# Performance work log

Measured on AMD Instinct MI355X. Metric: run time of the kernel, lower is better.

Reference implementation:

```python
import jax, jax.numpy as jnp
import numpy as np

B, S, D, H, DO, E, K = 4, 2048, 1024, 4096, 1024, 8, 2


def setup_inputs() -> dict:
    key = jax.random.key(0)
    ks = jax.random.split(key, 5)
    sD = 1.0 / np.sqrt(D)
    sH = 1.0 / np.sqrt(H)
    return {
        "x": jax.random.normal(ks[0], (B, S, D), jnp.float32),
        "gate_w": jax.random.normal(ks[1], (D, E), jnp.float32) * sD,
        "gate_b": jnp.zeros((E,), jnp.float32),
        "w1": jax.random.normal(ks[2], (E, D, H), jnp.float32) * sD,
        "b1": jnp.zeros((E, H), jnp.float32),
        "w2": jax.random.normal(ks[3], (E, H, DO), jnp.float32) * sH,
        "b2": jnp.zeros((E, DO), jnp.float32),
    }


def reference(x, gate_w, gate_b, w1, b1, w2, b2):
    # Eval mode: no gating noise, dropout is identity.
    T = B * S
    xf = x.reshape(T, D)
    logits = xf @ gate_w + gate_b                      # [T, E]
    top_v, top_i = jax.lax.top_k(logits, K)            # [T, K]
    top_w = jax.nn.softmax(top_v, axis=-1)             # softmax over top-k scores
    # scatter top-k weights into dense [T, E] gate weights (indices are distinct)
    weights = jnp.zeros_like(logits).at[jnp.arange(T)[:, None], top_i].set(top_w)
    # dense per-expert MLP, combined with (mostly zero) gate weights —
    # same math as the masked gather/scatter loop in the torch source
    h = jax.nn.relu(jnp.einsum('td,edh->teh', xf, w1) + b1)   # [T, E, H]
    eo = jnp.einsum('teh,eho->teo', h, w2) + b2               # [T, E, DO]
    out = jnp.einsum('te,teo->to', weights, eo).reshape(B, S, DO)
    expert_usage = jnp.bincount(top_i.reshape(-1), length=E)
    return out, weights, expert_usage, top_i
```

## Files before the change

kernel.cpp:

```cpp
#include <hip/hip_runtime.h>
#include <cstdint>
#include <cstddef>

typedef unsigned short u16;
typedef unsigned int u32;
typedef short s16x8 __attribute__((ext_vector_type(8)));
typedef float f32x4 __attribute__((ext_vector_type(4)));

#define T_TOK 8192
#define D_IN  1024
#define H_DIM 4096
#define DO_DIM 1024

__device__ __forceinline__ u16 f2bf(float f) {
    u32 u = __float_as_uint(f);
    return (u16)((u + 0x7FFFu + ((u >> 16) & 1u)) >> 16);
}

__device__ __forceinline__ f32x4 mfma16(s16x8 a, s16x8 b, f32x4 c) {
    return __builtin_amdgcn_mfma_f32_16x16x32_bf16(a, b, c, 0, 0, 0);
}

__device__ __forceinline__ void gload16(const void* g, void* l) {
    __builtin_amdgcn_global_load_lds(
        (const __attribute__((address_space(1))) void*)g,
        (__attribute__((address_space(3))) void*)l,
        16, 0, 0);
}

__global__ __launch_bounds__(256) void gate_kernel(
    const float* __restrict__ x, const float* __restrict__ gw,
    const float* __restrict__ gb, float* __restrict__ weights_out,
    float* __restrict__ topi_out, int* __restrict__ gcounts,
    int* __restrict__ tok_list, int* __restrict__ slot_of_tok)
{
    const int wid = threadIdx.x >> 6;
    const int lane = threadIdx.x & 63;
    const int tbase = blockIdx.x << 4;
    __shared__ int lcount[8];
    __shared__ int gbase[8];
    __shared__ short tinfo[16][4];
    if (threadIdx.x < 8) lcount[threadIdx.x] = 0;
    __syncthreads();

    for (int j = 0; j < 4; ++j) {
        const int t = tbase + (wid << 2) + j;
        const float* xr = x + ((size_t)t << 10);
        float p[8];
#pragma unroll
        for (int e = 0; e < 8; ++e) p[e] = 0.f;
#pragma unroll
        for (int i = 0; i < 16; ++i) {
            int d = lane + i * 64;
            float xv = xr[d];
            const f32x4 g0 = *(const f32x4*)(gw + d * 8);
            const f32x4 g1 = *(const f32x4*)(gw + d * 8 + 4);
            p[0] += xv * g0[0]; p[1] += xv * g0[1]; p[2] += xv * g0[2]; p[3] += xv * g0[3];
            p[4] += xv * g1[0]; p[5] += xv * g1[1]; p[6] += xv * g1[2]; p[7] += xv * g1[3];
        }
#pragma unroll
        for (int off = 32; off >= 1; off >>= 1) {
#pragma unroll
            for (int e = 0; e < 8; ++e) p[e] += __shfl_xor(p[e], off, 64);
        }
        if (lane == 0) {
            float lg[8];
#pragma unroll
            for (int e = 0; e < 8; ++e) lg[e] = p[e] + gb[e];
            int i0 = 0;
            for (int e = 1; e < 8; ++e) if (lg[e] > lg[i0]) i0 = e;
            int i1 = (i0 == 0) ? 1 : 0;
            for (int e = 0; e < 8; ++e) if (e != i0 && lg[e] > lg[i1]) i1 = e;
            float ex = expf(lg[i1] - lg[i0]);
            float p0 = 1.f / (1.f + ex);
            float p1 = ex / (1.f + ex);
#pragma unroll
            for (int e = 0; e < 8; ++e)
                weights_out[t * 8 + e] = (e == i0) ? p0 : ((e == i1) ? p1 : 0.f);
            topi_out[t * 2 + 0] = (float)i0;
            topi_out[t * 2 + 1] = (float)i1;
            int idx = (wid << 2) + j;
            int r0 = atomicAdd(&lcount[i0], 1);
            int r1 = atomicAdd(&lcount[i1], 1);
            tinfo[idx][0] = (short)i0; tinfo[idx][1] = (short)r0;
            tinfo[idx][2] = (short)i1; tinfo[idx][3] = (short)r1;
        }
    }
    __syncthreads();
    if (threadIdx.x < 8)
        gbase[threadIdx.x] = atomicAdd(&gcounts[threadIdx.x * 32], lcount[threadIdx.x]);
    __syncthreads();
    if (threadIdx.x < 16) {
        int t = tbase + threadIdx.x;
        int i0 = tinfo[threadIdx.x][0], r0 = tinfo[threadIdx.x][1];
        int i1 = tinfo[threadIdx.x][2], r1 = tinfo[threadIdx.x][3];
        int pos0 = gbase[i0] + r0;
        int pos1 = gbase[i1] + r1;
        tok_list[(i0 << 13) + pos0] = t;
        slot_of_tok[t * 2 + 0] = (i0 << 13) | pos0;
        tok_list[(i1 << 13) + pos1] = t;
        slot_of_tok[t * 2 + 1] = (i1 << 13) | pos1;
    }
}

__global__ void zero_counts_kernel(int* c) { c[threadIdx.x] = 0; }

__global__ void scan_kernel(const int* __restrict__ gcounts, int* __restrict__ counts,
                            int* __restrict__ base, float* __restrict__ usage_out,
                            int* __restrict__ rbt) {
    if (threadIdx.x == 0) {
        int acc = 0;
        for (int e = 0; e < 8; ++e) {
            int c = gcounts[e * 32];
            counts[e] = c;
            base[e] = acc;
            acc += c;
            usage_out[e] = (float)c;
        }
        int nrb = 0;
        for (int e = 0; e < 8; ++e) {
            int nb = (counts[e] + 127) >> 7;
            for (int rb = 0; rb < nb; ++rb) rbt[1 + nrb++] = (e << 16) | rb;
        }
        rbt[0] = nrb;
    }
}

__global__ __launch_bounds__(256) void gather_kernel(
    const float* __restrict__ x, const int* __restrict__ slot_of_tok,
    const int* __restrict__ base, u16* __restrict__ xg)
{
    const int t = blockIdx.x;
    const int s = slot_of_tok[t * 2 + blockIdx.y];
    const int slot = base[s >> 13] + (s & 8191);
    const int d = threadIdx.x * 4;
    float4 v = *(const float4*)(x + ((size_t)t << 10) + d);
    ushort4 h;
    h.x = f2bf(v.x); h.y = f2bf(v.y); h.z = f2bf(v.z); h.w = f2bf(v.w);
    *(ushort4*)(xg + ((size_t)slot << 10) + d) = h;
}

__global__ __launch_bounds__(256) void transpose_kernel(
    const float* __restrict__ w1, const float* __restrict__ w2,
    u16* __restrict__ w1t, u16* __restrict__ w2t, int chunk, int HC)
{
    const int e = blockIdx.z;
    const int tid = threadIdx.x;
    const int tiles_h = HC >> 6;
    const int ntile1 = 16 * tiles_h;
    int b = blockIdx.x;
    const float* src; u16* dst;
    size_t sstride, dstride;
    int r0, c0;
    if (b < ntile1) {
        int tr = b / tiles_h, tc = b % tiles_h;
        r0 = tr * 64; c0 = tc * 64;
        src = w1 + (size_t)e * D_IN * H_DIM + (size_t)chunk * HC;
        sstride = H_DIM;
        dst = w1t + (size_t)e * HC * D_IN;
        dstride = D_IN;
    } else {
        int tb = b - ntile1;
        int tr = tb / 16, tc = tb % 16;
        r0 = tr * 64; c0 = tc * 64;
        src = w2 + ((size_t)e * H_DIM + (size_t)chunk * HC) * DO_DIM;
        sstride = DO_DIM;
        dst = w2t + (size_t)e * DO_DIM * HC;
        dstride = HC;
    }
    __shared__ u16 tile[64][68];
#pragma unroll
    for (int i = 0; i < 4; ++i) {
        int flat = i * 1024 + tid * 4;
        int rr = flat >> 6, cc = flat & 63;
        float4 v = *(const float4*)(src + (size_t)(r0 + rr) * sstride + c0 + cc);
        ushort4 h4;
        h4.x = f2bf(v.x); h4.y = f2bf(v.y); h4.z = f2bf(v.z); h4.w = f2bf(v.w);
        *(ushort4*)&tile[rr][cc] = h4;
    }
    __syncthreads();
#pragma unroll
    for (int i = 0; i < 4; ++i) {
        int flat = i * 1024 + tid * 4;
        int rr = flat >> 6, cc = flat & 63;
        ushort4 o;
        o.x = tile[cc + 0][rr]; o.y = tile[cc + 1][rr];
        o.z = tile[cc + 2][rr]; o.w = tile[cc + 3][rr];
        *(ushort4*)(dst + (size_t)(c0 + rr) * dstride + r0 + cc) = o;
    }
}


__device__ __forceinline__ void stage6s(const char* const gA[2], const char* const gB[4],
                                        char* slab, int koff, int tid) {
    char* l = slab + __builtin_amdgcn_readfirstlane((tid >> 6) << 10);
#pragma unroll
    for (int i = 0; i < 2; ++i) gload16(gA[i] + koff, l + i * 8192);
#pragma unroll
    for (int i = 0; i < 4; ++i) gload16(gB[i] + koff, l + 16384 + i * 8192);
}

#define GEMM_CORE(NTV) \
    const int arow = (wm << 6) + (lane & 15); \
    const int brow = (wn << 6) + (lane & 15); \
    const int ko = (lane >> 4) << 4; \
    const int aoff0 = arow * 128 + (ko ^ ((arow & 7) << 4)); \
    const int aoff1 = arow * 128 + ((64 + ko) ^ ((arow & 7) << 4)); \
    const int boff0 = 16384 + brow * 128 + (ko ^ ((brow & 7) << 4)); \
    const int boff1 = 16384 + brow * 128 + ((64 + ko) ^ ((brow & 7) << 4)); \
    f32x4 acc[4][4]; \
    _Pragma("unroll") \
    for (int m = 0; m < 4; ++m) \
        _Pragma("unroll") \
        for (int n = 0; n < 4; ++n) acc[m][n] = f32x4{0.f, 0.f, 0.f, 0.f}; \
    stage6s(gA, gB, sm, 0, tid); \
    stage6s(gA, gB, sm + 49152, 128, tid); \
    int cs = 0; \
    _Pragma("unroll 1") \
    for (int t = 0; t < (NTV); ++t) { \
        if (t + 1 < (NTV)) asm volatile("s_waitcnt vmcnt(6)" ::: "memory"); \
        else               asm volatile("s_waitcnt vmcnt(0)" ::: "memory"); \
        __builtin_amdgcn_sched_barrier(0); \
        __builtin_amdgcn_s_barrier(); \
        __builtin_amdgcn_sched_barrier(0); \
        if (t + 2 < (NTV)) { \
            int ss = cs + 2; if (ss >= 3) ss -= 3; \
            stage6s(gA, gB, sm + ss * 49152, (t + 2) * 128, tid); \
        } \
        const char* S = sm + cs * 49152; \
        s16x8 la0[4], lb0[4], la1[4], lb1[4]; \
        _Pragma("unroll") \
        for (int m = 0; m < 4; ++m) la0[m] = *(const s16x8*)(S + aoff0 + m * 2048); \
        _Pragma("unroll") \
        for (int n = 0; n < 4; ++n) lb0[n] = *(const s16x8*)(S + boff0 + n * 2048); \
        _Pragma("unroll") \
        for (int m = 0; m < 4; ++m) la1[m] = *(const s16x8*)(S + aoff1 + m * 2048); \
        _Pragma("unroll") \
        for (int n = 0; n < 4; ++n) lb1[n] = *(const s16x8*)(S + boff1 + n * 2048); \
        __builtin_amdgcn_s_setprio(1); \
        _Pragma("unroll") \
        for (int m = 0; m < 4; ++m) \
            _Pragma("unroll") \
            for (int n = 0; n < 4; ++n) acc[m][n] = mfma16(la0[m], lb0[n], acc[m][n]); \
        _Pragma("unroll") \
        for (int m = 0; m < 4; ++m) \
            _Pragma("unroll") \
            for (int n = 0; n < 4; ++n) acc[m][n] = mfma16(la1[m], lb1[n], acc[m][n]); \
        __builtin_amdgcn_s_setprio(0); \
        cs = cs + 1; if (cs == 3) cs = 0; \
    }

__global__ __launch_bounds__(512) void gemm1_kernel(
    const u16* __restrict__ xg, const u16* __restrict__ w1t,
    const float* __restrict__ b1, u16* __restrict__ hbuf,
    const int* __restrict__ counts, const int* __restrict__ base,
    const int* __restrict__ rbt, int chunk, int HC)
{
    const int nrb = rbt[0];
    if (blockIdx.y >= nrb) return;
    const int ent = rbt[1 + blockIdx.y];
    const int e = ent >> 16;
    const int row0 = (ent & 0xffff) << 7;
    const int n_e = counts[e];
    const int sbase = base[e];
    const int col0 = blockIdx.x << 8;
    const int tid = threadIdx.x;
    const int lane = tid & 63;
    const int wv = tid >> 6;
    const int wm = wv >> 2;
    const int wn = wv & 3;

    __shared__ char sm[147456];

    const int srow_ = tid >> 3;
    const int scb_  = ((tid & 7) << 4) ^ ((srow_ & 7) << 4);
    const char* gA[2]; const char* gB[4];
#pragma unroll
    for (int i = 0; i < 2; ++i) {
        int slot = sbase + row0 + i * 64 + srow_;
        slot = slot < 16383 ? slot : 16383;
        gA[i] = (const char*)xg + ((size_t)slot << 11) + scb_;
    }
#pragma unroll
    for (int i = 0; i < 4; ++i) {
        int hrow = col0 + i * 64 + srow_;
        gB[i] = (const char*)w1t + (((size_t)e * HC + hrow) << 11) + scb_;
    }

    GEMM_CORE(16)

    const int crow = (wm << 6) + ((lane >> 4) << 2);
    const int ccol = (wn << 6) + (lane & 15);
    float bias_n[4];
#pragma unroll
    for (int n = 0; n < 4; ++n)
        bias_n[n] = b1[(e << 12) + chunk * HC + col0 + ccol + n * 16];
#pragma unroll
    for (int m = 0; m < 4; ++m) {
#pragma unroll
        for (int j = 0; j < 4; ++j) {
            int r = row0 + crow + m * 16 + j;
            if (r < n_e) {
                u16* dst = hbuf + (size_t)(sbase + r) * HC + col0;
#pragma unroll
                for (int n = 0; n < 4; ++n) {
                    float v = acc[m][n][j] + bias_n[n];
                    v = v > 0.f ? v : 0.f;
                    dst[ccol + n * 16] = f2bf(v);
                }
            }
        }
    }
}

__global__ __launch_bounds__(512) void gemm2_kernel(
    const u16* __restrict__ hbuf, const u16* __restrict__ w2t,
    const float* __restrict__ b2, float* __restrict__ eo,
    const int* __restrict__ counts, const int* __restrict__ base,
    const int* __restrict__ rbt, int chunk, int HC)
{
    const int nrb = rbt[0];
    if (blockIdx.y >= nrb) return;
    const int ent = rbt[1 + blockIdx.y];
    const int e = ent >> 16;
    const int row0 = (ent & 0xffff) << 7;
    const int n_e = counts[e];
    const int sbase = base[e];
    const int col0 = blockIdx.x << 8;
    const int tid = threadIdx.x;
    const int lane = tid & 63;
    const int wv = tid >> 6;
    const int wm = wv >> 2;
    const int wn = wv & 3;

    __shared__ char sm[147456];

    const int srow_ = tid >> 3;
    const int scb_  = ((tid & 7) << 4) ^ ((srow_ & 7) << 4);
    const char* gA[2]; const char* gB[4];
#pragma unroll
    for (int i = 0; i < 2; ++i) {
        int slot = sbase + row0 + i * 64 + srow_;
        slot = slot < 16383 ? slot : 16383;
        gA[i] = (const char*)hbuf + (((size_t)slot * HC) << 1) + scb_;
    }
#pragma unroll
    for (int i = 0; i < 4; ++i) {
        int orow = col0 + i * 64 + srow_;
        gB[i] = (const char*)w2t + ((((size_t)(e << 10) + orow) * HC) << 1) + scb_;
    }

    const int NT = HC >> 6;
    GEMM_CORE(NT)

    const int crow = (wm << 6) + ((lane >> 4) << 2);
    const int ccol = (wn << 6) + (lane & 15);
    float bias_n[4];
#pragma unroll
    for (int n = 0; n < 4; ++n)
        bias_n[n] = (chunk == 0) ? b2[(e << 10) + col0 + ccol + n * 16] : 0.f;
#pragma unroll
    for (int m = 0; m < 4; ++m) {
#pragma unroll
        for (int j = 0; j < 4; ++j) {
            int r = row0 + crow + m * 16 + j;
            if (r < n_e) {
                float* dst = eo + ((size_t)(sbase + r) << 10) + col0;
#pragma unroll
                for (int n = 0; n < 4; ++n) {
                    int c = ccol + n * 16;
                    float v = acc[m][n][j] + bias_n[n];
                    if (chunk) v += dst[c];
                    dst[c] = v;
                }
            }
        }
    }
}

__global__ __launch_bounds__(256) void combine_kernel(
    const float* __restrict__ eo, const float* __restrict__ weights,
    const int* __restrict__ slot_of_tok, const int* __restrict__ base,
    float* __restrict__ out)
{
    const int t = blockIdx.x;
    const int tid = threadIdx.x;
    int s0 = slot_of_tok[t * 2], s1 = slot_of_tok[t * 2 + 1];
    int e0 = s0 >> 13, e1 = s1 >> 13;
    int c0 = base[e0] + (s0 & 8191);
    int c1 = base[e1] + (s1 & 8191);
    float w0 = weights[t * 8 + e0];
    float w1 = weights[t * 8 + e1];
    int c = tid * 4;
    f32x4 a = *(const f32x4*)(eo + ((size_t)c0 << 10) + c);
    f32x4 b = *(const f32x4*)(eo + ((size_t)c1 << 10) + c);
    f32x4 r;
    r[0] = w0 * a[0] + w1 * b[0];
    r[1] = w0 * a[1] + w1 * b[1];
    r[2] = w0 * a[2] + w1 * b[2];
    r[3] = w0 * a[3] + w1 * b[3];
    *(f32x4*)(out + ((size_t)t << 10) + c) = r;
}

extern "C" void kernel_launch(void* const* d_in, const int* in_sizes, int n_in,
                              void* d_out, int out_size, void* d_ws, size_t ws_size,
                              hipStream_t stream)
{
    const float* x      = (const float*)d_in[0];
    const float* gate_w = (const float*)d_in[1];
    const float* gate_b = (const float*)d_in[2];
    const float* w1     = (const float*)d_in[3];
    const float* b1     = (const float*)d_in[4];
    const float* w2     = (const float*)d_in[5];
    const float* b2     = (const float*)d_in[6];

    float* out         = (float*)d_out;
    float* weights_out = out + (size_t)T_TOK * DO_DIM;
    float* usage_out   = weights_out + (size_t)T_TOK * 8;
    float* topi_out    = usage_out + 8;

    char* p = (char*)d_ws;
    int* gcounts = (int*)p;      p += 1024;
    int* counts = (int*)p;       p += 256;
    int* base   = (int*)p;       p += 256;
    int* rbt    = (int*)p;       p += 1024;
    int* tok_list = (int*)p;     p += (size_t)8 * 8192 * 4;
    int* slot_of_tok = (int*)p;  p += (size_t)8192 * 2 * 4;
    const size_t fixed = (size_t)(p - (char*)d_ws);

    const size_t xg_bytes = (size_t)16384 * 1024 * 2;
    const size_t eo_bytes = (size_t)16384 * 1024 * 4;
    int HC;
    if      (ws_size >= fixed + xg_bytes + eo_bytes + (size_t)65536 * 4096) HC = 4096;
    else if (ws_size >= fixed + xg_bytes + eo_bytes + (size_t)65536 * 2048) HC = 2048;
    else if (ws_size >= fixed + xg_bytes + eo_bytes + (size_t)65536 * 1024) HC = 1024;
    else                                                                    HC = 512;

    u16* xg   = (u16*)p; p += xg_bytes;
    u16* w1t  = (u16*)p; p += (size_t)8 * HC * 1024 * 2;
    u16* w2t  = (u16*)p; p += (size_t)8 * 1024 * HC * 2;
    u16* hbuf = (u16*)p; p += (size_t)16384 * HC * 2;
    float* eo = (float*)p;

    zero_counts_kernel<<<1, 256, 0, stream>>>(gcounts);
    gate_kernel<<<T_TOK / 16, 256, 0, stream>>>(x, gate_w, gate_b, weights_out, topi_out,
                                                gcounts, tok_list, slot_of_tok);
    scan_kernel<<<1, 64, 0, stream>>>(gcounts, counts, base, usage_out, rbt);
    gather_kernel<<<dim3(T_TOK, 2), 256, 0, stream>>>(x, slot_of_tok, base, xg);

    const int NC = H_DIM / HC;
    for (int c = 0; c < NC; ++c) {
        int tiles_h = HC / 64;
        transpose_kernel<<<dim3(2 * 16 * tiles_h, 1, 8), 256, 0, stream>>>(w1, w2, w1t, w2t, c, HC);
        gemm1_kernel<<<dim3(HC / 256, 136, 1), 512, 0, stream>>>(xg, w1t, b1, hbuf,
                                                                 counts, base, rbt, c, HC);
        gemm2_kernel<<<dim3(DO_DIM / 256, 136, 1), 512, 0, stream>>>(hbuf, w2t, b2, eo,
                                                                     counts, base, rbt, c, HC);
    }
    combine_kernel<<<T_TOK, 256, 0, stream>>>(eo, weights_out, slot_of_tok, base, out);
}
```

Baseline: 513.2 us.

## Fuse token gather into GEMM1 A-loads and merge gating with weight transpose

GEMM1 now reads fp32 activation rows directly from x through tok_list, converts them to bf16 in registers and writes them into LDS. This replaces the separate gather kernel and the bf16 xg buffer. The gate kernel and the first-chunk weight transpose are merged into one launch, with the block index choosing the role. This removes a kernel launch and the round trip of gathered activations through memory. The cost is a GEMM1 pipeline that mixes register-staged A loads with async B loads, reads twice the A bytes in fp32, and needs hand-tuned waitcnt values.

```diff
diff --git a/kernel.cpp b/kernel.cpp
--- a/kernel.cpp
+++ b/kernel.cpp
@@ -15,6 +15,15 @@
 __device__ __forceinline__ u16 f2bf(float f) {
     u32 u = __float_as_uint(f);
     return (u16)((u + 0x7FFFu + ((u >> 16) & 1u)) >> 16);
+}
+
+__device__ __forceinline__ s16x8 pack8(float4 a, float4 b) {
+    s16x8 r;
+    r[0] = (short)f2bf(a.x); r[1] = (short)f2bf(a.y);
+    r[2] = (short)f2bf(a.z); r[3] = (short)f2bf(a.w);
+    r[4] = (short)f2bf(b.x); r[5] = (short)f2bf(b.y);
+    r[6] = (short)f2bf(b.z); r[7] = (short)f2bf(b.w);
+    return r;
 }
 
 __device__ __forceinline__ f32x4 mfma16(s16x8 a, s16x8 b, f32x4 c) {
@@ -28,127 +37,95 @@
         16, 0, 0);
 }
 
-__global__ __launch_bounds__(256) void gate_kernel(
+__global__ __launch_bounds__(256) void gate_transpose_kernel(
     const float* __restrict__ x, const float* __restrict__ gw,
     const float* __restrict__ gb, float* __restrict__ weights_out,
     float* __restrict__ topi_out, int* __restrict__ gcounts,
-    int* __restrict__ tok_list, int* __restrict__ slot_of_tok)
+    int* __restrict__ tok_list, int* __restrict__ slot_of_tok,
+    const float* __restrict__ w1, const float* __restrict__ w2,
+    u16* __restrict__ w1t, u16* __restrict__ w2t,
+    int chunk, int HC, int gate_blocks)
 {
-    const int wid = threadIdx.x >> 6;
-    const int lane = threadIdx.x & 63;
-    const int tbase = blockIdx.x << 4;
+    __shared__ u16 tile[64][68];
     __shared__ int lcount[8];
     __shared__ int gbase[8];
     __shared__ short tinfo[16][4];
-    if (threadIdx.x < 8) lcount[threadIdx.x] = 0;
-    __syncthreads();
-
-    for (int j = 0; j < 4; ++j) {
-        const int t = tbase + (wid << 2) + j;
-        const float* xr = x + ((size_t)t << 10);
-        float p[8];
-#pragma unroll
-        for (int e = 0; e < 8; ++e) p[e] = 0.f;
-#pragma unroll
-        for (int i = 0; i < 16; ++i) {
-            int d = lane + i * 64;
-            float xv = xr[d];
-            const f32x4 g0 = *(const f32x4*)(gw + d * 8);
-            const f32x4 g1 = *(const f32x4*)(gw + d * 8 + 4);
-            p[0] += xv * g0[0]; p[1] += xv * g0[1]; p[2] += xv * g0[2]; p[3] += xv * g0[3];
-            p[4] += xv * g1[0]; p[5] += xv * g1[1]; p[6] += xv * g1[2]; p[7] += xv * g1[3];
-        }
-#pragma unroll
-        for (int off = 32; off >= 1; off >>= 1) {
-#pragma unroll
-            for (int e = 0; e < 8; ++e) p[e] += __shfl_xor(p[e], off, 64);
-        }
-        if (lane == 0) {
-            float lg[8];
-#pragma unroll
-            for (int e = 0; e < 8; ++e) lg[e] = p[e] + gb[e];
-            int i0 = 0;
-            for (int e = 1; e < 8; ++e) if (lg[e] > lg[i0]) i0 = e;
-            int i1 = (i0 == 0) ? 1 : 0;
-            for (int e = 0; e < 8; ++e) if (e != i0 && lg[e] > lg[i1]) i1 = e;
-            float ex = expf(lg[i1] - lg[i0]);
-            float p0 = 1.f / (1.f + ex);
-            float p1 = ex / (1.f + ex);
-#pragma unroll
-            for (int e = 0; e < 8; ++e)
-                weights_out[t * 8 + e] = (e == i0) ? p0 : ((e == i1) ? p1 : 0.f);
-            topi_out[t * 2 + 0] = (float)i0;
-            topi_out[t * 2 + 1] = (float)i1;
-            int idx = (wid << 2) + j;
-            int r0 = atomicAdd(&lcount[i0], 1);
-            int r1 = atomicAdd(&lcount[i1], 1);
-            tinfo[idx][0] = (short)i0; tinfo[idx][1] = (short)r0;
-            tinfo[idx][2] = (short)i1; tinfo[idx][3] = (short)r1;
-        }
-    }
-    __syncthreads();
-    if (threadIdx.x < 8)
-        gbase[threadIdx.x] = atomicAdd(&gcounts[threadIdx.x * 32], lcount[threadIdx.x]);
-    __syncthreads();
-    if (threadIdx.x < 16) {
-        int t = tbase + threadIdx.x;
-        int i0 = tinfo[threadIdx.x][0], r0 = tinfo[threadIdx.x][1];
-        int i1 = tinfo[threadIdx.x][2], r1 = tinfo[threadIdx.x][3];
-        int pos0 = gbase[i0] + r0;
-        int pos1 = gbase[i1] + r1;
-        tok_list[(i0 << 13) + pos0] = t;
-        slot_of_tok[t * 2 + 0] = (i0 << 13) | pos0;
-        tok_list[(i1 << 13) + pos1] = t;
-        slot_of_tok[t * 2 + 1] = (i1 << 13) | pos1;
-    }
-}
-
-__global__ void zero_counts_kernel(int* c) { c[threadIdx.x] = 0; }
-
-__global__ void scan_kernel(const int* __restrict__ gcounts, int* __restrict__ counts,
-                            int* __restrict__ base, float* __restrict__ usage_out,
-                            int* __restrict__ rbt) {
-    if (threadIdx.x == 0) {
-        int acc = 0;
-        for (int e = 0; e < 8; ++e) {
-            int c = gcounts[e * 32];
-            counts[e] = c;
-            base[e] = acc;
-            acc += c;
-            usage_out[e] = (float)c;
-        }
-        int nrb = 0;
-        for (int e = 0; e < 8; ++e) {
-            int nb = (counts[e] + 127) >> 7;
-            for (int rb = 0; rb < nb; ++rb) rbt[1 + nrb++] = (e << 16) | rb;
-        }
-        rbt[0] = nrb;
-    }
-}
-
-__global__ __launch_bounds__(256) void gather_kernel(
-    const float* __restrict__ x, const int* __restrict__ slot_of_tok,
-    const int* __restrict__ base, u16* __restrict__ xg)
-{
-    const int t = blockIdx.x;
-    const int s = slot_of_tok[t * 2 + blockIdx.y];
-    const int slot = base[s >> 13] + (s & 8191);
-    const int d = threadIdx.x * 4;
-    float4 v = *(const float4*)(x + ((size_t)t << 10) + d);
-    ushort4 h;
-    h.x = f2bf(v.x); h.y = f2bf(v.y); h.z = f2bf(v.z); h.w = f2bf(v.w);
-    *(ushort4*)(xg + ((size_t)slot << 10) + d) = h;
-}
-
-__global__ __launch_bounds__(256) void transpose_kernel(
-    const float* __restrict__ w1, const float* __restrict__ w2,
-    u16* __restrict__ w1t, u16* __restrict__ w2t, int chunk, int HC)
-{
-    const int e = blockIdx.z;
+
+    const int bid = blockIdx.x;
+    if (bid < gate_blocks) {
+        const int wid = threadIdx.x >> 6;
+        const int lane = threadIdx.x & 63;
+        const int tbase = bid << 4;
+        if (threadIdx.x < 8) lcount[threadIdx.x] = 0;
+        __syncthreads();
+        for (int j = 0; j < 4; ++j) {
+            const int t = tbase + (wid << 2) + j;
+            const float* xr = x + ((size_t)t << 10);
+            float p[8];
+#pragma unroll
+            for (int e = 0; e < 8; ++e) p[e] = 0.f;
+#pragma unroll
+            for (int i = 0; i < 16; ++i) {
+                int d = lane + i * 64;
+                float xv = xr[d];
+                const f32x4 g0 = *(const f32x4*)(gw + d * 8);
+                const f32x4 g1 = *(const f32x4*)(gw + d * 8 + 4);
+                p[0] += xv * g0[0]; p[1] += xv * g0[1]; p[2] += xv * g0[2]; p[3] += xv * g0[3];
+                p[4] += xv * g1[0]; p[5] += xv * g1[1]; p[6] += xv * g1[2]; p[7] += xv * g1[3];
+            }
+#pragma unroll
+            for (int off = 32; off >= 1; off >>= 1) {
+#pragma unroll
+                for (int e = 0; e < 8; ++e) p[e] += __shfl_xor(p[e], off, 64);
+            }
+            if (lane == 0) {
+                float lg[8];
+#pragma unroll
+                for (int e = 0; e < 8; ++e) lg[e] = p[e] + gb[e];
+                int i0 = 0;
+                for (int e = 1; e < 8; ++e) if (lg[e] > lg[i0]) i0 = e;
+                int i1 = (i0 == 0) ? 1 : 0;
+                for (int e = 0; e < 8; ++e) if (e != i0 && lg[e] > lg[i1]) i1 = e;
+                float ex = expf(lg[i1] - lg[i0]);
+                float p0 = 1.f / (1.f + ex);
+                float p1 = ex / (1.f + ex);
+#pragma unroll
+                for (int e = 0; e < 8; ++e)
+                    weights_out[t * 8 + e] = (e == i0) ? p0 : ((e == i1) ? p1 : 0.f);
+                topi_out[t * 2 + 0] = (float)i0;
+                topi_out[t * 2 + 1] = (float)i1;
+                int idx = (wid << 2) + j;
+                int r0 = atomicAdd(&lcount[i0], 1);
+                int r1 = atomicAdd(&lcount[i1], 1);
+                tinfo[idx][0] = (short)i0; tinfo[idx][1] = (short)r0;
+                tinfo[idx][2] = (short)i1; tinfo[idx][3] = (short)r1;
+            }
+        }
+        __syncthreads();
+        if (threadIdx.x < 8)
+            gbase[threadIdx.x] = atomicAdd(&gcounts[threadIdx.x * 32], lcount[threadIdx.x]);
+        __syncthreads();
+        if (threadIdx.x < 16) {
+            int t = tbase + threadIdx.x;
+            int i0 = tinfo[threadIdx.x][0], r0 = tinfo[threadIdx.x][1];
+            int i1 = tinfo[threadIdx.x][2], r1 = tinfo[threadIdx.x][3];
+            int pos0 = gbase[i0] + r0;
+            int pos1 = gbase[i1] + r1;
+            tok_list[(i0 << 13) + pos0] = t;
+            slot_of_tok[t * 2 + 0] = (i0 << 13) | pos0;
+            tok_list[(i1 << 13) + pos1] = t;
+            slot_of_tok[t * 2 + 1] = (i1 << 13) | pos1;
+        }
+        return;
+    }
+
     const int tid = threadIdx.x;
     const int tiles_h = HC >> 6;
+    const int per_e = 32 * tiles_h;
     const int ntile1 = 16 * tiles_h;
-    int b = blockIdx.x;
+    const int b2 = bid - gate_blocks;
+    const int e = b2 / per_e;
+    const int b = b2 - e * per_e;
     const float* src; u16* dst;
     size_t sstride, dstride;
     int r0, c0;
@@ -168,7 +145,6 @@
         dst = w2t + (size_t)e * DO_DIM * HC;
         dstride = HC;
     }
-    __shared__ u16 tile[64][68];
 #pragma unroll
     for (int i = 0; i < 4; ++i) {
         int flat = i * 1024 + tid * 4;
@@ -190,6 +166,29 @@
     }
 }
 
+__global__ void zero_counts_kernel(int* c) { c[threadIdx.x] = 0; }
+
+__global__ void scan_kernel(const int* __restrict__ gcounts, int* __restrict__ counts,
+                            int* __restrict__ base, float* __restrict__ usage_out,
+                            int* __restrict__ rbt) {
+    if (threadIdx.x == 0) {
+        int acc = 0;
+        for (int e = 0; e < 8; ++e) {
+            int c = gcounts[e * 32];
+            counts[e] = c;
+            base[e] = acc;
+            acc += c;
+            usage_out[e] = (float)c;
+        }
+        int nrb = 0;
+        for (int e = 0; e < 8; ++e) {
+            int nb = (counts[e] + 127) >> 7;
+            for (int rb = 0; rb < nb; ++rb) rbt[1 + nrb++] = (e << 16) | rb;
+        }
+        rbt[0] = nrb;
+    }
+}
+
 
 __device__ __forceinline__ void stage6s(const char* const gA[2], const char* const gB[4],
                                         char* slab, int koff, int tid) {
@@ -200,61 +199,60 @@
     for (int i = 0; i < 4; ++i) gload16(gB[i] + koff, l + 16384 + i * 8192);
 }
 
-#define GEMM_CORE(NTV) \
-    const int arow = (wm << 6) + (lane & 15); \
-    const int brow = (wn << 6) + (lane & 15); \
-    const int ko = (lane >> 4) << 4; \
-    const int aoff0 = arow * 128 + (ko ^ ((arow & 7) << 4)); \
-    const int aoff1 = arow * 128 + ((64 + ko) ^ ((arow & 7) << 4)); \
-    const int boff0 = 16384 + brow * 128 + (ko ^ ((brow & 7) << 4)); \
-    const int boff1 = 16384 + brow * 128 + ((64 + ko) ^ ((brow & 7) << 4)); \
-    f32x4 acc[4][4]; \
+#define MFMA_BLOCK(S) do { \
+    s16x8 la0[4], lb0[4], la1[4], lb1[4]; \
+    _Pragma("unroll") \
+    for (int m = 0; m < 4; ++m) la0[m] = *(const s16x8*)((S) + aoff0 + m * 2048); \
+    _Pragma("unroll") \
+    for (int n = 0; n < 4; ++n) lb0[n] = *(const s16x8*)((S) + boff0 + n * 2048); \
+    _Pragma("unroll") \
+    for (int m = 0; m < 4; ++m) la1[m] = *(const s16x8*)((S) + aoff1 + m * 2048); \
+    _Pragma("unroll") \
+    for (int n = 0; n < 4; ++n) lb1[n] = *(const s16x8*)((S) + boff1 + n * 2048); \
+    __builtin_amdgcn_s_setprio(1); \
     _Pragma("unroll") \
     for (int m = 0; m < 4; ++m) \
         _Pragma("unroll") \
-        for (int n = 0; n < 4; ++n) acc[m][n] = f32x4{0.f, 0.f, 0.f, 0.f}; \
-    stage6s(gA, gB, sm, 0, tid); \
-    stage6s(gA, gB, sm + 49152, 128, tid); \
-    int cs = 0; \
-    _Pragma("unroll 1") \
-    for (int t = 0; t < (NTV); ++t) { \
-        if (t + 1 < (NTV)) asm volatile("s_waitcnt vmcnt(6)" ::: "memory"); \
-        else               asm volatile("s_waitcnt vmcnt(0)" ::: "memory"); \
-        __builtin_amdgcn_sched_barrier(0); \
-        __builtin_amdgcn_s_barrier(); \
-        __builtin_amdgcn_sched_barrier(0); \
-        if (t + 2 < (NTV)) { \
-            int ss = cs + 2; if (ss >= 3) ss -= 3; \
-            stage6s(gA, gB, sm + ss * 49152, (t + 2) * 128, tid); \
-        } \
-        const char* S = sm + cs * 49152; \
-        s16x8 la0[4], lb0[4], la1[4], lb1[4]; \
+        for (int n = 0; n < 4; ++n) acc[m][n] = mfma16(la0[m], lb0[n], acc[m][n]); \
+    _Pragma("unroll") \
+    for (int m = 0; m < 4; ++m) \
         _Pragma("unroll") \
-        for (int m = 0; m < 4; ++m) la0[m] = *(const s16x8*)(S + aoff0 + m * 2048); \
-        _Pragma("unroll") \
-        for (int n = 0; n < 4; ++n) lb0[n] = *(const s16x8*)(S + boff0 + n * 2048); \
-        _Pragma("unroll") \
-        for (int m = 0; m < 4; ++m) la1[m] = *(const s16x8*)(S + aoff1 + m * 2048); \
-        _Pragma("unroll") \
-        for (int n = 0; n < 4; ++n) lb1[n] = *(const s16x8*)(S + boff1 + n * 2048); \
-        __builtin_amdgcn_s_setprio(1); \
-        _Pragma("unroll") \
-        for (int m = 0; m < 4; ++m) \
-            _Pragma("unroll") \
-            for (int n = 0; n < 4; ++n) acc[m][n] = mfma16(la0[m], lb0[n], acc[m][n]); \
-        _Pragma("unroll") \
-        for (int m = 0; m < 4; ++m) \
-            _Pragma("unroll") \
-            for (int n = 0; n < 4; ++n) acc[m][n] = mfma16(la1[m], lb1[n], acc[m][n]); \
-        __builtin_amdgcn_s_setprio(0); \
-        cs = cs + 1; if (cs == 3) cs = 0; \
-    }
+        for (int n = 0; n < 4; ++n) acc[m][n] = mfma16(la1[m], lb1[n], acc[m][n]); \
+    __builtin_amdgcn_s_setprio(0); } while(0)
+
+#define G1BODY(TAU, LD, CV) do { \
+    if ((TAU) + 1 < 16) asm volatile("s_waitcnt vmcnt(4)" ::: "memory"); \
+    else                asm volatile("s_waitcnt vmcnt(0)" ::: "memory"); \
+    asm volatile("s_waitcnt lgkmcnt(0)" ::: "memory"); \
+    __builtin_amdgcn_sched_barrier(0); \
+    __builtin_amdgcn_s_barrier(); \
+    __builtin_amdgcn_sched_barrier(0); \
+    int s1_ = cs + 1; if (s1_ == 3) s1_ = 0; \
+    int s2_ = cs + 2; if (s2_ >= 3) s2_ -= 3; \
+    if ((TAU) + 2 < 16) { \
+        const int ka_ = ((TAU) + 2) << 8; \
+        LD##0 = *(const float4*)(gAx0 + ka_);      LD##1 = *(const float4*)(gAx0 + ka_ + 16); \
+        LD##2 = *(const float4*)(gAx1 + ka_);      LD##3 = *(const float4*)(gAx1 + ka_ + 16); \
+        const int kb_ = ((TAU) + 2) << 7; \
+        char* l_ = sm + s2_ * 49152 + 16384 + wofs; \
+        gload16(gB[0] + kb_, l_);           gload16(gB[1] + kb_, l_ + 8192); \
+        gload16(gB[2] + kb_, l_ + 16384);   gload16(gB[3] + kb_, l_ + 24576); \
+    } \
+    if ((TAU) + 1 < 16) { \
+        char* sw_ = sm + s1_ * 49152; \
+        *(s16x8*)(sw_ + wA0) = pack8(CV##0, CV##1); \
+        *(s16x8*)(sw_ + wA1) = pack8(CV##2, CV##3); \
+    } \
+    const char* S_ = sm + cs * 49152; \
+    MFMA_BLOCK(S_); \
+    cs = s1_; } while(0)
 
 __global__ __launch_bounds__(512) void gemm1_kernel(
-    const u16* __restrict__ xg, const u16* __restrict__ w1t,
+    const float* __restrict__ x, const u16* __restrict__ w1t,
     const float* __restrict__ b1, u16* __restrict__ hbuf,
     const int* __restrict__ counts, const int* __restrict__ base,
-    const int* __restrict__ rbt, int chunk, int HC)
+    const int* __restrict__ rbt, const int* __restrict__ tok_list,
+    int chunk, int HC)
 {
     const int nrb = rbt[0];
     if (blockIdx.y >= nrb) return;
@@ -272,22 +270,63 @@
 
     __shared__ char sm[147456];
 
-    const int srow_ = tid >> 3;
-    const int scb_  = ((tid & 7) << 4) ^ ((srow_ & 7) << 4);
-    const char* gA[2]; const char* gB[4];
-#pragma unroll
-    for (int i = 0; i < 2; ++i) {
-        int slot = sbase + row0 + i * 64 + srow_;
-        slot = slot < 16383 ? slot : 16383;
-        gA[i] = (const char*)xg + ((size_t)slot << 11) + scb_;
-    }
+    const int r0_ = tid >> 3;
+    const int r1_ = r0_ + 64;
+    const int kseg = tid & 7;
+    int row_a0 = row0 + r0_; row_a0 = row_a0 < n_e ? row_a0 : n_e - 1;
+    int row_a1 = row0 + r1_; row_a1 = row_a1 < n_e ? row_a1 : n_e - 1;
+    const int tk0 = tok_list[(e << 13) + row_a0];
+    const int tk1 = tok_list[(e << 13) + row_a1];
+    const char* gAx0 = (const char*)x + ((size_t)tk0 << 12) + (kseg << 5);
+    const char* gAx1 = (const char*)x + ((size_t)tk1 << 12) + (kseg << 5);
+    const int wA0 = r0_ * 128 + ((kseg << 4) ^ ((r0_ & 7) << 4));
+    const int wA1 = r1_ * 128 + ((kseg << 4) ^ ((r1_ & 7) << 4));
+
+    const int scb_ = ((tid & 7) << 4) ^ (((tid >> 3) & 7) << 4);
+    const char* gB[4];
 #pragma unroll
     for (int i = 0; i < 4; ++i) {
-        int hrow = col0 + i * 64 + srow_;
+        int hrow = col0 + i * 64 + (tid >> 3);
         gB[i] = (const char*)w1t + (((size_t)e * HC + hrow) << 11) + scb_;
     }
-
-    GEMM_CORE(16)
+    const int wofs = __builtin_amdgcn_readfirstlane((tid >> 6) << 10);
+
+    const int arow = (wm << 6) + (lane & 15);
+    const int brow = (wn << 6) + (lane & 15);
+    const int ko = (lane >> 4) << 4;
+    const int aoff0 = arow * 128 + (ko ^ ((arow & 7) << 4));
+    const int aoff1 = arow * 128 + ((64 + ko) ^ ((arow & 7) << 4));
+    const int boff0 = 16384 + brow * 128 + (ko ^ ((brow & 7) << 4));
+    const int boff1 = 16384 + brow * 128 + ((64 + ko) ^ ((brow & 7) << 4));
+
+    f32x4 acc[4][4];
+#pragma unroll
+    for (int m = 0; m < 4; ++m)
+#pragma unroll
+        for (int n = 0; n < 4; ++n) acc[m][n] = f32x4{0.f, 0.f, 0.f, 0.f};
+
+    float4 aE0, aE1, aE2, aE3, aO0, aO1, aO2, aO3;
+
+    aE0 = *(const float4*)(gAx0);       aE1 = *(const float4*)(gAx0 + 16);
+    aE2 = *(const float4*)(gAx1);       aE3 = *(const float4*)(gAx1 + 16);
+    {   char* l_ = sm + 16384 + wofs;
+        gload16(gB[0], l_);           gload16(gB[1], l_ + 8192);
+        gload16(gB[2], l_ + 16384);   gload16(gB[3], l_ + 24576); }
+    aO0 = *(const float4*)(gAx0 + 256); aO1 = *(const float4*)(gAx0 + 272);
+    aO2 = *(const float4*)(gAx1 + 256); aO3 = *(const float4*)(gAx1 + 272);
+    {   char* l_ = sm + 49152 + 16384 + wofs;
+        gload16(gB[0] + 128, l_);           gload16(gB[1] + 128, l_ + 8192);
+        gload16(gB[2] + 128, l_ + 16384);   gload16(gB[3] + 128, l_ + 24576); }
+    asm volatile("s_waitcnt vmcnt(12)" ::: "memory");
+    *(s16x8*)(sm + wA0) = pack8(aE0, aE1);
+    *(s16x8*)(sm + wA1) = pack8(aE2, aE3);
+
+    int cs = 0;
+#pragma unroll 1
+    for (int tt = 0; tt < 16; tt += 2) {
+        G1BODY(tt, aE, aO);
+        G1BODY(tt + 1, aO, aE);
+    }
 
     const int crow = (wm << 6) + ((lane >> 4) << 2);
     const int ccol = (wn << 6) + (lane & 15);
@@ -335,23 +374,56 @@
 
     __shared__ char sm[147456];
 
-    const int srow_ = tid >> 3;
-    const int scb_  = ((tid & 7) << 4) ^ ((srow_ & 7) << 4);
+    const int scb_ = ((tid & 7) << 4) ^ (((tid >> 3) & 7) << 4);
     const char* gA[2]; const char* gB[4];
 #pragma unroll
     for (int i = 0; i < 2; ++i) {
-        int slot = sbase + row0 + i * 64 + srow_;
+        int slot = sbase + row0 + i * 64 + (tid >> 3);
         slot = slot < 16383 ? slot : 16383;
         gA[i] = (const char*)hbuf + (((size_t)slot * HC) << 1) + scb_;
     }
 #pragma unroll
     for (int i = 0; i < 4; ++i) {
-        int orow = col0 + i * 64 + srow_;
+        int orow = col0 + i * 64 + (tid >> 3);
         gB[i] = (const char*)w2t + ((((size_t)(e << 10) + orow) * HC) << 1) + scb_;
     }
+    const int wofs = __builtin_amdgcn_readfirstlane((tid >> 6) << 10);
+    (void)wofs;
+
+    const int arow = (wm << 6) + (lane & 15);
+    const int brow = (wn << 6) + (lane & 15);
+    const int ko = (lane >> 4) << 4;
+    const int aoff0 = arow * 128 + (ko ^ ((arow & 7) << 4));
+    const int aoff1 = arow * 128 + ((64 + ko) ^ ((arow & 7) << 4));
+    const int boff0 = 16384 + brow * 128 + (ko ^ ((brow & 7) << 4));
+    const int boff1 = 16384 + brow * 128 + ((64 + ko) ^ ((brow & 7) << 4));
+
+    f32x4 acc[4][4];
+#pragma unroll
+    for (int m = 0; m < 4; ++m)
+#pragma unroll
+        for (int n = 0; n < 4; ++n) acc[m][n] = f32x4{0.f, 0.f, 0.f, 0.f};
 
     const int NT = HC >> 6;
-    GEMM_CORE(NT)
+    stage6s(gA, gB, sm, 0, tid);
+    stage6s(gA, gB, sm + 49152, 128, tid);
+
+    int cs = 0;
+#pragma unroll 1
+    for (int t = 0; t < NT; ++t) {
+        if (t + 1 < NT) asm volatile("s_waitcnt vmcnt(6)" ::: "memory");
+        else            asm volatile("s_waitcnt vmcnt(0)" ::: "memory");
+        __builtin_amdgcn_sched_barrier(0);
+        __builtin_amdgcn_s_barrier();
+        __builtin_amdgcn_sched_barrier(0);
+        if (t + 2 < NT) {
+            int ss = cs + 2; if (ss >= 3) ss -= 3;
+            stage6s(gA, gB, sm + ss * 49152, (t + 2) * 128, tid);
+        }
+        const char* S_ = sm + cs * 49152;
+        MFMA_BLOCK(S_);
+        cs = cs + 1; if (cs == 3) cs = 0;
+    }
 
     const int crow = (wm << 6) + ((lane >> 4) << 2);
     const int ccol = (wn << 6) + (lane & 15);
@@ -428,32 +500,37 @@
     int* slot_of_tok = (int*)p;  p += (size_t)8192 * 2 * 4;
     const size_t fixed = (size_t)(p - (char*)d_ws);
 
-    const size_t xg_bytes = (size_t)16384 * 1024 * 2;
     const size_t eo_bytes = (size_t)16384 * 1024 * 4;
     int HC;
-    if      (ws_size >= fixed + xg_bytes + eo_bytes + (size_t)65536 * 4096) HC = 4096;
-    else if (ws_size >= fixed + xg_bytes + eo_bytes + (size_t)65536 * 2048) HC = 2048;
-    else if (ws_size >= fixed + xg_bytes + eo_bytes + (size_t)65536 * 1024) HC = 1024;
-    else                                                                    HC = 512;
-
-    u16* xg   = (u16*)p; p += xg_bytes;
+    if      (ws_size >= fixed + eo_bytes + (size_t)65536 * 4096) HC = 4096;
+    else if (ws_size >= fixed + eo_bytes + (size_t)65536 * 2048) HC = 2048;
+    else if (ws_size >= fixed + eo_bytes + (size_t)65536 * 1024) HC = 1024;
+    else                                                         HC = 512;
+
     u16* w1t  = (u16*)p; p += (size_t)8 * HC * 1024 * 2;
     u16* w2t  = (u16*)p; p += (size_t)8 * 1024 * HC * 2;
     u16* hbuf = (u16*)p; p += (size_t)16384 * HC * 2;
     float* eo = (float*)p;
 
+    const int tiles_h = HC / 64;
+    const int per_e = 32 * tiles_h;
+    const int trans_blocks = 8 * per_e;
+
     zero_counts_kernel<<<1, 256, 0, stream>>>(gcounts);
-    gate_kernel<<<T_TOK / 16, 256, 0, stream>>>(x, gate_w, gate_b, weights_out, topi_out,
-                                                gcounts, tok_list, slot_of_tok);
+    gate_transpose_kernel<<<512 + trans_blocks, 256, 0, stream>>>(
+        x, gate_w, gate_b, weights_out, topi_out, gcounts, tok_list, slot_of_tok,
+        w1, w2, w1t, w2t, 0, HC, 512);
     scan_kernel<<<1, 64, 0, stream>>>(gcounts, counts, base, usage_out, rbt);
-    gather_kernel<<<dim3(T_TOK, 2), 256, 0, stream>>>(x, slot_of_tok, base, xg);
 
     const int NC = H_DIM / HC;
     for (int c = 0; c < NC; ++c) {
-        int tiles_h = HC / 64;
-        transpose_kernel<<<dim3(2 * 16 * tiles_h, 1, 8), 256, 0, stream>>>(w1, w2, w1t, w2t, c, HC);
-        gemm1_kernel<<<dim3(HC / 256, 136, 1), 512, 0, stream>>>(xg, w1t, b1, hbuf,
-                                                                 counts, base, rbt, c, HC);
+        if (c > 0)
+            gate_transpose_kernel<<<trans_blocks, 256, 0, stream>>>(
+                x, gate_w, gate_b, weights_out, topi_out, gcounts, tok_list, slot_of_tok,
+                w1, w2, w1t, w2t, c, HC, 0);
+        gemm1_kernel<<<dim3(HC / 256, 136, 1), 512, 0, stream>>>(x, w1t, b1, hbuf,
+                                                                 counts, base, rbt, tok_list,
+                                                                 c, HC);
         gemm2_kernel<<<dim3(DO_DIM / 256, 136, 1), 512, 0, stream>>>(hbuf, w2t, b2, eo,
                                                                      counts, base, rbt, c, HC);
     }
```

Measured after the change: 616.4 us. 20.1% more time.
